# Kernel tuning notes

Measured on AMD Instinct MI355X. Metric: run time of the kernel, lower is better.

The kernel has to match this reference:

```python
import jax, jax.numpy as jnp
import numpy as np

E = 256
H = 512
LN_EPS = 1e-5
NORM_EPS = 1e-12


def setup_inputs() -> dict:
    key = jax.random.key(0)
    ks = jax.random.split(key, 8)
    B, N, M = 8, 128, 128
    track_features = jax.random.normal(ks[0], (B, N, E), dtype=jnp.float32)
    det_features = jax.random.normal(ks[1], (B, M, E), dtype=jnp.float32)
    # MLP params (torch Linear default init style: uniform, but values irrelevant for correctness harness)
    lim1 = 1.0 / np.sqrt(3 * E)
    W1 = jax.random.uniform(ks[2], (3 * E, H), minval=-lim1, maxval=lim1, dtype=jnp.float32)
    b1 = jax.random.uniform(ks[3], (H,), minval=-lim1, maxval=lim1, dtype=jnp.float32)
    gamma = jnp.ones((H,), dtype=jnp.float32)
    beta = jnp.zeros((H,), dtype=jnp.float32)
    lim2 = 1.0 / np.sqrt(H)
    W2 = jax.random.uniform(ks[4], (H, 1), minval=-lim2, maxval=lim2, dtype=jnp.float32)
    b2 = jax.random.uniform(ks[5], (1,), minval=-lim2, maxval=lim2, dtype=jnp.float32)
    return {"track_features": track_features, "det_features": det_features,
            "W1": W1, "b1": b1, "gamma": gamma, "beta": beta, "W2": W2, "b2": b2}


def _l2_normalize(x):
    # F.normalize(x, dim=-1): x / max(||x||_2, eps)
    n = jnp.sqrt(jnp.sum(x * x, axis=-1, keepdims=True))
    return x / jnp.maximum(n, NORM_EPS)


def reference(track_features, det_features, W1, b1, gamma, beta, W2, b2):
    t = _l2_normalize(track_features)   # (B, N, E)
    d = _l2_normalize(det_features)     # (B, M, E)
    tb = t[:, :, None, :]               # (B, N, 1, E)
    db = d[:, None, :, :]               # (B, 1, M, E)
    B, N, _ = t.shape
    M = d.shape[1]
    diff = jnp.abs(tb - db)                                  # (B, N, M, E)
    pair = jnp.concatenate([jnp.broadcast_to(tb, (B, N, M, E)),
                            jnp.broadcast_to(db, (B, N, M, E)),
                            diff], axis=-1)                  # (B, N, M, 3E)
    h = jnp.einsum('bnme,eh->bnmh', pair, W1) + b1           # (B, N, M, H)
    mu = jnp.mean(h, axis=-1, keepdims=True)
    var = jnp.mean((h - mu) ** 2, axis=-1, keepdims=True)
    h = (h - mu) * jax.lax.rsqrt(var + LN_EPS) * gamma + beta
    h = h * jax.nn.sigmoid(h)                                # SiLU
    out = jnp.einsum('bnmh,ho->bnmo', h, W2)[..., 0] + b2[0]  # (B, N, M)
    return out
```

## Files before the change

### kernel.cpp

```cpp
#include <hip/hip_runtime.h>
#include <hip/hip_bf16.h>
#include <cstdint>

typedef __bf16 bf16x8 __attribute__((ext_vector_type(8)));
typedef __bf16 bf16x2 __attribute__((ext_vector_type(2)));
typedef float f32x4 __attribute__((ext_vector_type(4)));

#define E_DIM 256
#define H_DIM 512
#define TSTR 260

static __device__ __forceinline__ unsigned pkbf(float a, float b) {
    bf16x2 h;
    h[0] = (__bf16)a;
    h[1] = (__bf16)b;
    return __builtin_bit_cast(unsigned, h);
}

__global__ __launch_bounds__(256)
void w1conv_kernel(const float* __restrict__ W1, __bf16* __restrict__ W1cc) {
    int u = blockIdx.x * 256 + threadIdx.x;
    int j   = u & 3;
    int h   = (u >> 2) & 511;
    int c   = (u >> 11) & 7;
    int mat = u >> 14;
    const float* src = W1 + (size_t)(mat * 256 + c * 32 + j * 8) * H_DIM + h;
    uint4 v;
    v.x = pkbf(src[0], src[(size_t)1 * H_DIM]);
    v.y = pkbf(src[(size_t)2 * H_DIM], src[(size_t)3 * H_DIM]);
    v.z = pkbf(src[(size_t)4 * H_DIM], src[(size_t)5 * H_DIM]);
    v.w = pkbf(src[(size_t)6 * H_DIM], src[(size_t)7 * H_DIM]);
    *(uint4*)(W1cc + ((size_t)(mat * 8 + c) * 512 + h) * 32 + j * 8) = v;
}

__global__ __launch_bounds__(512, 4)
void pq_mfma_kernel(const float* __restrict__ track, const float* __restrict__ det,
                    const __bf16* __restrict__ W1cc, const float* __restrict__ b1,
                    float* __restrict__ P, float* __restrict__ Q) {
    __shared__ __align__(16) __bf16 Ash[32 * 256];
    __shared__ float sclS[32];

    int tid  = threadIdx.x;
    int lane = tid & 63;
    int wave = tid >> 6;
    int lq   = lane >> 4;
    int lc   = lane & 15;

    int blk  = blockIdx.x;
    int mat  = blk >> 6;
    int rowg = (blk >> 1) & 31;
    int half = blk & 1;
    int r0   = rowg * 32;
    int h0   = half * 256;
    const float* src = mat ? det : track;

#pragma unroll
    for (int i = 0; i < 4; ++i) {
        int row = wave * 4 + i;
        float4 x = ((const float4*)(src + (size_t)(r0 + row) * E_DIM))[lane];
        float ss = x.x*x.x + x.y*x.y + x.z*x.z + x.w*x.w;
#pragma unroll
        for (int off = 32; off > 0; off >>= 1) ss += __shfl_xor(ss, off);
        if (lane == 0) sclS[row] = 1.0f / fmaxf(sqrtf(ss), 1e-12f);
    }
    __syncthreads();

#pragma unroll
    for (int r = 0; r < 2; ++r) {
        int row = r * 16 + lc;
        float st = sclS[row];
        const float* gp = src + (size_t)(r0 + row) * E_DIM + wave * 32 + lq * 8;
        float4 t0 = *(const float4*)gp;
        float4 t1 = *(const float4*)(gp + 4);
        uint4 v;
        v.x = pkbf(t0.x * st, t0.y * st);
        v.y = pkbf(t0.z * st, t0.w * st);
        v.z = pkbf(t1.x * st, t1.y * st);
        v.w = pkbf(t1.z * st, t1.w * st);
        *(uint4*)&Ash[(size_t)(r * 512 + wave * 64 + lane) * 8] = v;
    }
    __syncthreads();

    const uint4* Wg = (const uint4*)W1cc + (mat ? 16384 : 0);
    int hb = h0 + wave * 32 + lc;
    bf16x8 bwA[2], bwB[2];
#pragma unroll
    for (int ht = 0; ht < 2; ++ht)
        bwA[ht] = __builtin_bit_cast(bf16x8, Wg[(hb + ht * 16) * 4 + lq]);

    f32x4 acc[2][2];
#pragma unroll
    for (int pt = 0; pt < 2; ++pt)
#pragma unroll
        for (int ht = 0; ht < 2; ++ht)
            acc[pt][ht] = (f32x4){0.f, 0.f, 0.f, 0.f};

#pragma unroll 2
    for (int c = 0; c < 8; ++c) {
        bf16x8* cur = (c & 1) ? bwB : bwA;
        bf16x8* nxt = (c & 1) ? bwA : bwB;
        int c1 = (c + 1) & 7;
#pragma unroll
        for (int ht = 0; ht < 2; ++ht)
            nxt[ht] = __builtin_bit_cast(bf16x8, Wg[c1 * 2048 + (hb + ht * 16) * 4 + lq]);
#pragma unroll
        for (int pt = 0; pt < 2; ++pt) {
            bf16x8 af = *(const bf16x8*)&Ash[(size_t)((pt * 8 + c) * 64 + lane) * 8];
#pragma unroll
            for (int ht = 0; ht < 2; ++ht)
                acc[pt][ht] = __builtin_amdgcn_mfma_f32_16x16x32_bf16(cur[ht], af, acc[pt][ht], 0, 0, 0);
        }
    }

    float* dst = mat ? Q : P;
#pragma unroll
    for (int ht = 0; ht < 2; ++ht) {
        int h = h0 + wave * 32 + ht * 16 + lq * 4;
        f32x4 bvv = (f32x4){0.f, 0.f, 0.f, 0.f};
        if (!mat) bvv = *(const f32x4*)&b1[h];
#pragma unroll
        for (int pt = 0; pt < 2; ++pt) {
            f32x4 o = acc[pt][ht] + bvv;
            *(f32x4*)&dst[(size_t)(r0 + pt * 16 + lc) * H_DIM + h] = o;
        }
    }
}

__global__ __launch_bounds__(512, 4)
void main_kernel(const float* __restrict__ track, const float* __restrict__ det,
                 const __bf16* __restrict__ W1cc,
                 const float* __restrict__ P, const float* __restrict__ Q,
                 const float* __restrict__ gamma, const float* __restrict__ beta,
                 const float* __restrict__ W2, const float* __restrict__ b2,
                 float* __restrict__ out) {
    __shared__ __align__(16) char SMEM[49408];
    __bf16* Ash  = (__bf16*)SMEM;
    float*  tsl  = (float*)(SMEM + 32768);
    float*  dsl  = (float*)(SMEM + 41088);
    float*  LNr1 = (float*)(SMEM + 32768);
    float*  LNr2 = (float*)(SMEM + 35072);
    float*  Red2 = (float*)(SMEM + 37376);
    float*  MuS  = (float*)(SMEM + 39680);
    float*  RsS  = (float*)(SMEM + 39936);
    __shared__ float sclT[8], sclD[8];

    int tid  = threadIdx.x;
    int lane = tid & 63;
    int wave = tid >> 6;
    int lq   = lane >> 4;
    int lc   = lane & 15;

    int blk = blockIdx.x;
    int b   = blk >> 8;
    int n0  = ((blk >> 4) & 15) * 8;
    int m0  = (blk & 15) * 8;

    float4 tstage = ((const float4*)(track + (size_t)(b * 128 + n0 + wave) * E_DIM))[lane];
    float4 dstage = ((const float4*)(det   + (size_t)(b * 128 + m0 + wave) * E_DIM))[lane];

    const uint4* Wg = (const uint4*)W1cc + 32768;
    int hb = wave * 64 + lc;
    bf16x8 bwA[4], bwB[4];
#pragma unroll
    for (int ht = 0; ht < 4; ++ht)
        bwA[ht] = __builtin_bit_cast(bf16x8, Wg[(hb + ht * 16) * 4 + lq]);

    {
        float a = tstage.x*tstage.x + tstage.y*tstage.y + tstage.z*tstage.z + tstage.w*tstage.w;
        float d = dstage.x*dstage.x + dstage.y*dstage.y + dstage.z*dstage.z + dstage.w*dstage.w;
#pragma unroll
        for (int off = 32; off > 0; off >>= 1) { a += __shfl_xor(a, off); d += __shfl_xor(d, off); }
        if (lane == 0) {
            sclT[wave] = 1.0f / fmaxf(sqrtf(a), 1e-12f);
            sclD[wave] = 1.0f / fmaxf(sqrtf(d), 1e-12f);
        }
    }
    *(float4*)&tsl[wave * TSTR + lane * 4] = tstage;
    *(float4*)&dsl[wave * TSTR + lane * 4] = dstage;
    __syncthreads();

    {
        int k0 = wave * 32 + lq * 8;
        int ml = lane & 7;
        float sd = sclD[ml];
        const float* dr = dsl + ml * TSTR + k0;
        float4 d0 = *(const float4*)dr;
        float4 d1 = *(const float4*)(dr + 4);
#pragma unroll
        for (int r = 0; r < 4; ++r) {
            int nl = r * 2 + (lc >> 3);
            float st = sclT[nl];
            const float* tr = tsl + nl * TSTR + k0;
            float4 t0 = *(const float4*)tr;
            float4 t1 = *(const float4*)(tr + 4);
            uint4 v;
            v.x = pkbf(fabsf(t0.x * st - d0.x * sd), fabsf(t0.y * st - d0.y * sd));
            v.y = pkbf(fabsf(t0.z * st - d0.z * sd), fabsf(t0.w * st - d0.w * sd));
            v.z = pkbf(fabsf(t1.x * st - d1.x * sd), fabsf(t1.y * st - d1.y * sd));
            v.w = pkbf(fabsf(t1.z * st - d1.z * sd), fabsf(t1.w * st - d1.w * sd));
            *(uint4*)&Ash[(size_t)(r * 512 + wave * 64 + lane) * 8] = v;
        }
    }

    const float* Pb = P + (size_t)(b * 128 + n0) * H_DIM;
    const float* Qb = Q + (size_t)(b * 128 + m0) * H_DIM;
    f32x4 acc[4][4];
    {
        f32x4 qv[4];
#pragma unroll
        for (int ht = 0; ht < 4; ++ht)
            qv[ht] = *(const f32x4*)&Qb[(size_t)(lc & 7) * H_DIM + wave * 64 + ht * 16 + lq * 4];
#pragma unroll
        for (int pt = 0; pt < 4; ++pt) {
            int n = pt * 2 + (lc >> 3);
#pragma unroll
            for (int ht = 0; ht < 4; ++ht) {
                f32x4 pv = *(const f32x4*)&Pb[(size_t)n * H_DIM + wave * 64 + ht * 16 + lq * 4];
                acc[pt][ht] = pv + qv[ht];
            }
        }
    }
    __syncthreads();

#pragma unroll 2
    for (int c = 0; c < 8; ++c) {
        bf16x8* cur = (c & 1) ? bwB : bwA;
        bf16x8* nxt = (c & 1) ? bwA : bwB;
        int c1 = (c + 1) & 7;
#pragma unroll
        for (int ht = 0; ht < 4; ++ht)
            nxt[ht] = __builtin_bit_cast(bf16x8, Wg[c1 * 2048 + (hb + ht * 16) * 4 + lq]);
#pragma unroll
        for (int pt = 0; pt < 4; ++pt) {
            bf16x8 af = *(const bf16x8*)&Ash[(size_t)((pt * 8 + c) * 64 + lane) * 8];
#pragma unroll
            for (int ht = 0; ht < 4; ++ht)
                acc[pt][ht] = __builtin_amdgcn_mfma_f32_16x16x32_bf16(cur[ht], af, acc[pt][ht], 0, 0, 0);
        }
    }

#pragma unroll
    for (int pt = 0; pt < 4; ++pt) {
        float s1 = 0.f, s2 = 0.f;
#pragma unroll
        for (int ht = 0; ht < 4; ++ht)
#pragma unroll
            for (int rg = 0; rg < 4; ++rg) {
                float v = acc[pt][ht][rg];
                s1 += v; s2 += v * v;
            }
        s1 += __shfl_xor(s1, 16); s2 += __shfl_xor(s2, 16);
        s1 += __shfl_xor(s1, 32); s2 += __shfl_xor(s2, 32);
        if (lq == 0) {
            LNr1[(pt * 16 + lc) * 9 + wave] = s1;
            LNr2[(pt * 16 + lc) * 9 + wave] = s2;
        }
    }
    __syncthreads();
    if (tid < 64) {
        float S1 = 0.f, S2 = 0.f;
#pragma unroll
        for (int w = 0; w < 8; ++w) { S1 += LNr1[tid * 9 + w]; S2 += LNr2[tid * 9 + w]; }
        float mu = S1 * (1.0f / 512.0f);
        float var = S2 * (1.0f / 512.0f) - mu * mu;
        MuS[tid] = mu;
        RsS[tid] = rsqrtf(var + 1e-5f);
    }
    __syncthreads();

    float mus[4], rss[4];
#pragma unroll
    for (int pt = 0; pt < 4; ++pt) { mus[pt] = MuS[pt * 16 + lc]; rss[pt] = RsS[pt * 16 + lc]; }
    float ca[4] = {0.f, 0.f, 0.f, 0.f};
#pragma unroll
    for (int ht = 0; ht < 4; ++ht) {
        int h = wave * 64 + ht * 16 + lq * 4;
        f32x4 g  = *(const f32x4*)&gamma[h];
        f32x4 bb = *(const f32x4*)&beta[h];
        f32x4 w  = *(const f32x4*)&W2[h];
#pragma unroll
        for (int pt = 0; pt < 4; ++pt) {
#pragma unroll
            for (int rg = 0; rg < 4; ++rg) {
                float x = (acc[pt][ht][rg] - mus[pt]) * rss[pt] * g[rg] + bb[rg];
                float sg = __builtin_amdgcn_rcpf(1.0f + __expf(-x));
                ca[pt] += x * sg * w[rg];
            }
        }
    }
#pragma unroll
    for (int pt = 0; pt < 4; ++pt) {
        float c = ca[pt];
        c += __shfl_xor(c, 16);
        c += __shfl_xor(c, 32);
        if (lq == 0) Red2[(pt * 16 + lc) * 9 + wave] = c;
    }
    __syncthreads();
    if (tid < 64) {
        float o = b2[0];
#pragma unroll
        for (int w = 0; w < 8; ++w) o += Red2[tid * 9 + w];
        int n = n0 + (tid >> 3);
        int m = m0 + (tid & 7);
        out[(size_t)(b * 128 + n) * 128 + m] = o;
    }
}

extern "C" void kernel_launch(void* const* d_in, const int* in_sizes, int n_in,
                              void* d_out, int out_size, void* d_ws, size_t ws_size,
                              hipStream_t stream) {
    const float* track = (const float*)d_in[0];
    const float* det   = (const float*)d_in[1];
    const float* W1    = (const float*)d_in[2];
    const float* b1    = (const float*)d_in[3];
    const float* gamma = (const float*)d_in[4];
    const float* beta  = (const float*)d_in[5];
    const float* W2    = (const float*)d_in[6];
    const float* b2    = (const float*)d_in[7];
    float* out = (float*)d_out;

    char* ws = (char*)d_ws;
    float*  P     = (float*)(ws);
    float*  Q     = (float*)(ws + (2u << 20));
    __bf16* W1cc  = (__bf16*)(ws + (4u << 20));

    w1conv_kernel<<<192, 256, 0, stream>>>(W1, W1cc);
    pq_mfma_kernel<<<128, 512, 0, stream>>>(track, det, W1cc, b1, P, Q);
    main_kernel<<<2048, 512, 0, stream>>>(track, det, W1cc, P, Q, gamma, beta, W2, b2, out);
}
```

Baseline: 153.0 us.

## Switch main GEMM to 32x32x16 MFMA with new W1 diff-slice layout

Replaces the 16x16x32 bf16 MFMA tiling of the diff-feature GEMM with 32x32x16 MFMAs. A new W1 slice layout is added in the conversion kernel, and the LDS A-tile layout and accumulator mapping change to match. Normalization scales are applied before staging to LDS, so the diff build no longer reads per-row scales. The LN and output reductions are spread across all waves with shuffles instead of one wave looping. The larger MFMA should raise compute density and cut instruction count, at the cost of a deeper weight prefetch ring, more register pressure from f32x16 accumulators, and more conversion work.

Measured after the change: 163.4 us. 6.8% more time.

```diff
diff --git a/kernel.cpp b/kernel.cpp
--- a/kernel.cpp
+++ b/kernel.cpp
@@ -5,6 +5,7 @@
 typedef __bf16 bf16x8 __attribute__((ext_vector_type(8)));
 typedef __bf16 bf16x2 __attribute__((ext_vector_type(2)));
 typedef float f32x4 __attribute__((ext_vector_type(4)));
+typedef float f32x16 __attribute__((ext_vector_type(16)));
 
 #define E_DIM 256
 #define H_DIM 512
@@ -19,18 +20,37 @@
 
 __global__ __launch_bounds__(256)
 void w1conv_kernel(const float* __restrict__ W1, __bf16* __restrict__ W1cc) {
-    int u = blockIdx.x * 256 + threadIdx.x;
-    int j   = u & 3;
-    int h   = (u >> 2) & 511;
-    int c   = (u >> 11) & 7;
-    int mat = u >> 14;
-    const float* src = W1 + (size_t)(mat * 256 + c * 32 + j * 8) * H_DIM + h;
-    uint4 v;
-    v.x = pkbf(src[0], src[(size_t)1 * H_DIM]);
-    v.y = pkbf(src[(size_t)2 * H_DIM], src[(size_t)3 * H_DIM]);
-    v.z = pkbf(src[(size_t)4 * H_DIM], src[(size_t)5 * H_DIM]);
-    v.w = pkbf(src[(size_t)6 * H_DIM], src[(size_t)7 * H_DIM]);
-    *(uint4*)(W1cc + ((size_t)(mat * 8 + c) * 512 + h) * 32 + j * 8) = v;
+    int blk = blockIdx.x;
+    int tid = threadIdx.x;
+    if (blk < 128) {
+        int u = blk * 256 + tid;
+        int j   = u & 3;
+        int h   = (u >> 2) & 511;
+        int c   = (u >> 11) & 7;
+        int mat = u >> 14;
+        const float* src = W1 + (size_t)(mat * 256 + c * 32 + j * 8) * H_DIM + h;
+        uint4 v;
+        v.x = pkbf(src[0], src[(size_t)1 * H_DIM]);
+        v.y = pkbf(src[(size_t)2 * H_DIM], src[(size_t)3 * H_DIM]);
+        v.z = pkbf(src[(size_t)4 * H_DIM], src[(size_t)5 * H_DIM]);
+        v.w = pkbf(src[(size_t)6 * H_DIM], src[(size_t)7 * H_DIM]);
+        *(uint4*)(W1cc + ((size_t)(mat * 8 + c) * 512 + h) * 32 + j * 8) = v;
+    } else {
+        int v = (blk - 128) * 256 + tid;
+        int hh    = v & 31;
+        int k8    = (v >> 5) & 1;
+        int hgrp  = (v >> 6) & 15;
+        int kstep = v >> 10;
+        int h  = hgrp * 32 + hh;
+        int k0 = kstep * 16 + k8 * 8;
+        const float* src = W1 + (size_t)(512 + k0) * H_DIM + h;
+        uint4 o;
+        o.x = pkbf(src[0], src[(size_t)1 * H_DIM]);
+        o.y = pkbf(src[(size_t)2 * H_DIM], src[(size_t)3 * H_DIM]);
+        o.z = pkbf(src[(size_t)4 * H_DIM], src[(size_t)5 * H_DIM]);
+        o.w = pkbf(src[(size_t)6 * H_DIM], src[(size_t)7 * H_DIM]);
+        *(uint4*)(W1cc + 262144 + (size_t)v * 8) = o;
+    }
 }
 
 __global__ __launch_bounds__(512, 4)
@@ -142,13 +162,12 @@
     float*  Red2 = (float*)(SMEM + 37376);
     float*  MuS  = (float*)(SMEM + 39680);
     float*  RsS  = (float*)(SMEM + 39936);
-    __shared__ float sclT[8], sclD[8];
 
     int tid  = threadIdx.x;
     int lane = tid & 63;
     int wave = tid >> 6;
-    int lq   = lane >> 4;
-    int lc   = lane & 15;
+    int l32  = lane & 31;
+    int lh   = lane >> 5;
 
     int blk = blockIdx.x;
     int b   = blk >> 8;
@@ -158,151 +177,172 @@
     float4 tstage = ((const float4*)(track + (size_t)(b * 128 + n0 + wave) * E_DIM))[lane];
     float4 dstage = ((const float4*)(det   + (size_t)(b * 128 + m0 + wave) * E_DIM))[lane];
 
-    const uint4* Wg = (const uint4*)W1cc + 32768;
-    int hb = wave * 64 + lc;
-    bf16x8 bwA[4], bwB[4];
-#pragma unroll
-    for (int ht = 0; ht < 4; ++ht)
-        bwA[ht] = __builtin_bit_cast(bf16x8, Wg[(hb + ht * 16) * 4 + lq]);
+    const uint4* Wg2 = (const uint4*)W1cc + 32768;
+    bf16x8 bw[4][2];
+#pragma unroll
+    for (int ht = 0; ht < 2; ++ht) {
+        bw[0][ht] = __builtin_bit_cast(bf16x8, Wg2[(wave * 2 + ht) * 64 + lane]);
+        bw[1][ht] = __builtin_bit_cast(bf16x8, Wg2[(16 + wave * 2 + ht) * 64 + lane]);
+    }
 
     {
         float a = tstage.x*tstage.x + tstage.y*tstage.y + tstage.z*tstage.z + tstage.w*tstage.w;
         float d = dstage.x*dstage.x + dstage.y*dstage.y + dstage.z*dstage.z + dstage.w*dstage.w;
 #pragma unroll
         for (int off = 32; off > 0; off >>= 1) { a += __shfl_xor(a, off); d += __shfl_xor(d, off); }
-        if (lane == 0) {
-            sclT[wave] = 1.0f / fmaxf(sqrtf(a), 1e-12f);
-            sclD[wave] = 1.0f / fmaxf(sqrtf(d), 1e-12f);
-        }
+        float st = 1.0f / fmaxf(sqrtf(a), 1e-12f);
+        float sd = 1.0f / fmaxf(sqrtf(d), 1e-12f);
+        tstage.x *= st; tstage.y *= st; tstage.z *= st; tstage.w *= st;
+        dstage.x *= sd; dstage.y *= sd; dstage.z *= sd; dstage.w *= sd;
     }
     *(float4*)&tsl[wave * TSTR + lane * 4] = tstage;
     *(float4*)&dsl[wave * TSTR + lane * 4] = dstage;
     __syncthreads();
 
     {
-        int k0 = wave * 32 + lq * 8;
-        int ml = lane & 7;
-        float sd = sclD[ml];
-        const float* dr = dsl + ml * TSTR + k0;
-        float4 d0 = *(const float4*)dr;
-        float4 d1 = *(const float4*)(dr + 4);
-#pragma unroll
-        for (int r = 0; r < 4; ++r) {
-            int nl = r * 2 + (lc >> 3);
-            float st = sclT[nl];
-            const float* tr = tsl + nl * TSTR + k0;
-            float4 t0 = *(const float4*)tr;
-            float4 t1 = *(const float4*)(tr + 4);
+        int m   = l32;
+        int pt  = wave & 1;
+        int ks0 = wave >> 1;
+        int p   = pt * 32 + m;
+        const float* tr = tsl + (p >> 3) * TSTR;
+        const float* dr = dsl + (p & 7) * TSTR;
+#pragma unroll
+        for (int i = 0; i < 4; ++i) {
+            int kstep = i * 4 + ks0;
+            int k0 = kstep * 16 + lh * 8;
+            float4 t0 = *(const float4*)(tr + k0);
+            float4 t1 = *(const float4*)(tr + k0 + 4);
+            float4 d0 = *(const float4*)(dr + k0);
+            float4 d1 = *(const float4*)(dr + k0 + 4);
             uint4 v;
-            v.x = pkbf(fabsf(t0.x * st - d0.x * sd), fabsf(t0.y * st - d0.y * sd));
-            v.y = pkbf(fabsf(t0.z * st - d0.z * sd), fabsf(t0.w * st - d0.w * sd));
-            v.z = pkbf(fabsf(t1.x * st - d1.x * sd), fabsf(t1.y * st - d1.y * sd));
-            v.w = pkbf(fabsf(t1.z * st - d1.z * sd), fabsf(t1.w * st - d1.w * sd));
-            *(uint4*)&Ash[(size_t)(r * 512 + wave * 64 + lane) * 8] = v;
+            v.x = pkbf(fabsf(t0.x - d0.x), fabsf(t0.y - d0.y));
+            v.y = pkbf(fabsf(t0.z - d0.z), fabsf(t0.w - d0.w));
+            v.z = pkbf(fabsf(t1.x - d1.x), fabsf(t1.y - d1.y));
+            v.w = pkbf(fabsf(t1.z - d1.z), fabsf(t1.w - d1.w));
+            *(uint4*)&Ash[(size_t)(((kstep * 2 + pt) * 2 + lh) * 32 + m) * 8] = v;
         }
     }
 
     const float* Pb = P + (size_t)(b * 128 + n0) * H_DIM;
     const float* Qb = Q + (size_t)(b * 128 + m0) * H_DIM;
-    f32x4 acc[4][4];
-    {
-        f32x4 qv[4];
-#pragma unroll
-        for (int ht = 0; ht < 4; ++ht)
-            qv[ht] = *(const f32x4*)&Qb[(size_t)(lc & 7) * H_DIM + wave * 64 + ht * 16 + lq * 4];
-#pragma unroll
-        for (int pt = 0; pt < 4; ++pt) {
-            int n = pt * 2 + (lc >> 3);
-#pragma unroll
-            for (int ht = 0; ht < 4; ++ht) {
-                f32x4 pv = *(const f32x4*)&Pb[(size_t)n * H_DIM + wave * 64 + ht * 16 + lq * 4];
-                acc[pt][ht] = pv + qv[ht];
-            }
-        }
-    }
-    __syncthreads();
-
-#pragma unroll 2
-    for (int c = 0; c < 8; ++c) {
-        bf16x8* cur = (c & 1) ? bwB : bwA;
-        bf16x8* nxt = (c & 1) ? bwA : bwB;
-        int c1 = (c + 1) & 7;
-#pragma unroll
-        for (int ht = 0; ht < 4; ++ht)
-            nxt[ht] = __builtin_bit_cast(bf16x8, Wg[c1 * 2048 + (hb + ht * 16) * 4 + lq]);
-#pragma unroll
-        for (int pt = 0; pt < 4; ++pt) {
-            bf16x8 af = *(const bf16x8*)&Ash[(size_t)((pt * 8 + c) * 64 + lane) * 8];
-#pragma unroll
-            for (int ht = 0; ht < 4; ++ht)
-                acc[pt][ht] = __builtin_amdgcn_mfma_f32_16x16x32_bf16(cur[ht], af, acc[pt][ht], 0, 0, 0);
-        }
-    }
-
-#pragma unroll
-    for (int pt = 0; pt < 4; ++pt) {
+    f32x16 acc[2][2];
+    {
+        int mq = lane & 7;
+        f32x4 qv[2][4];
+#pragma unroll
+        for (int ht = 0; ht < 2; ++ht)
+#pragma unroll
+            for (int rq = 0; rq < 4; ++rq)
+                qv[ht][rq] = *(const f32x4*)&Qb[(size_t)mq * H_DIM + wave * 64 + ht * 32 + rq * 8 + lh * 4];
+#pragma unroll
+        for (int pt = 0; pt < 2; ++pt) {
+            int n = pt * 4 + (l32 >> 3);
+#pragma unroll
+            for (int ht = 0; ht < 2; ++ht)
+#pragma unroll
+                for (int rq = 0; rq < 4; ++rq) {
+                    f32x4 pv = *(const f32x4*)&Pb[(size_t)n * H_DIM + wave * 64 + ht * 32 + rq * 8 + lh * 4];
+                    f32x4 s = pv + qv[ht][rq];
+#pragma unroll
+                    for (int j = 0; j < 4; ++j) acc[pt][ht][rq * 4 + j] = s[j];
+                }
+        }
+    }
+    __syncthreads();
+
+#pragma unroll 4
+    for (int ks = 0; ks < 16; ++ks) {
+        if (ks < 14) {
+#pragma unroll
+            for (int ht = 0; ht < 2; ++ht)
+                bw[(ks + 2) & 3][ht] = __builtin_bit_cast(bf16x8,
+                    Wg2[((ks + 2) * 16 + wave * 2 + ht) * 64 + lane]);
+        }
+#pragma unroll
+        for (int pt = 0; pt < 2; ++pt) {
+            bf16x8 af = *(const bf16x8*)&Ash[(size_t)((ks * 2 + pt) * 64 + lane) * 8];
+#pragma unroll
+            for (int ht = 0; ht < 2; ++ht)
+                acc[pt][ht] = __builtin_amdgcn_mfma_f32_32x32x16_bf16(bw[ks & 3][ht], af, acc[pt][ht], 0, 0, 0);
+        }
+    }
+
+#pragma unroll
+    for (int pt = 0; pt < 2; ++pt) {
         float s1 = 0.f, s2 = 0.f;
 #pragma unroll
-        for (int ht = 0; ht < 4; ++ht)
-#pragma unroll
-            for (int rg = 0; rg < 4; ++rg) {
-                float v = acc[pt][ht][rg];
+        for (int ht = 0; ht < 2; ++ht)
+#pragma unroll
+            for (int r = 0; r < 16; ++r) {
+                float v = acc[pt][ht][r];
                 s1 += v; s2 += v * v;
             }
-        s1 += __shfl_xor(s1, 16); s2 += __shfl_xor(s2, 16);
         s1 += __shfl_xor(s1, 32); s2 += __shfl_xor(s2, 32);
-        if (lq == 0) {
-            LNr1[(pt * 16 + lc) * 9 + wave] = s1;
-            LNr2[(pt * 16 + lc) * 9 + wave] = s2;
-        }
-    }
-    __syncthreads();
-    if (tid < 64) {
-        float S1 = 0.f, S2 = 0.f;
-#pragma unroll
-        for (int w = 0; w < 8; ++w) { S1 += LNr1[tid * 9 + w]; S2 += LNr2[tid * 9 + w]; }
-        float mu = S1 * (1.0f / 512.0f);
-        float var = S2 * (1.0f / 512.0f) - mu * mu;
-        MuS[tid] = mu;
-        RsS[tid] = rsqrtf(var + 1e-5f);
-    }
-    __syncthreads();
-
-    float mus[4], rss[4];
-#pragma unroll
-    for (int pt = 0; pt < 4; ++pt) { mus[pt] = MuS[pt * 16 + lc]; rss[pt] = RsS[pt * 16 + lc]; }
-    float ca[4] = {0.f, 0.f, 0.f, 0.f};
-#pragma unroll
-    for (int ht = 0; ht < 4; ++ht) {
-        int h = wave * 64 + ht * 16 + lq * 4;
-        f32x4 g  = *(const f32x4*)&gamma[h];
-        f32x4 bb = *(const f32x4*)&beta[h];
-        f32x4 w  = *(const f32x4*)&W2[h];
-#pragma unroll
-        for (int pt = 0; pt < 4; ++pt) {
-#pragma unroll
-            for (int rg = 0; rg < 4; ++rg) {
-                float x = (acc[pt][ht][rg] - mus[pt]) * rss[pt] * g[rg] + bb[rg];
-                float sg = __builtin_amdgcn_rcpf(1.0f + __expf(-x));
-                ca[pt] += x * sg * w[rg];
+        if (lane < 32) {
+            LNr1[(pt * 32 + l32) * 9 + wave] = s1;
+            LNr2[(pt * 32 + l32) * 9 + wave] = s2;
+        }
+    }
+    __syncthreads();
+    {
+        int pair = wave * 8 + (lane >> 3);
+        int idx  = lane & 7;
+        float s1 = LNr1[pair * 9 + idx];
+        float s2 = LNr2[pair * 9 + idx];
+        s1 += __shfl_xor(s1, 1); s2 += __shfl_xor(s2, 1);
+        s1 += __shfl_xor(s1, 2); s2 += __shfl_xor(s2, 2);
+        s1 += __shfl_xor(s1, 4); s2 += __shfl_xor(s2, 4);
+        if ((lane & 7) == 0) {
+            float mu = s1 * (1.0f / 512.0f);
+            float var = s2 * (1.0f / 512.0f) - mu * mu;
+            MuS[pair] = mu;
+            RsS[pair] = rsqrtf(var + 1e-5f);
+        }
+    }
+    __syncthreads();
+
+    float mus[2], rss[2];
+#pragma unroll
+    for (int pt = 0; pt < 2; ++pt) { mus[pt] = MuS[pt * 32 + l32]; rss[pt] = RsS[pt * 32 + l32]; }
+    float ca[2] = {0.f, 0.f};
+#pragma unroll
+    for (int ht = 0; ht < 2; ++ht) {
+#pragma unroll
+        for (int rq = 0; rq < 4; ++rq) {
+            int h = wave * 64 + ht * 32 + rq * 8 + lh * 4;
+            f32x4 g  = *(const f32x4*)&gamma[h];
+            f32x4 bb = *(const f32x4*)&beta[h];
+            f32x4 w  = *(const f32x4*)&W2[h];
+#pragma unroll
+            for (int pt = 0; pt < 2; ++pt) {
+#pragma unroll
+                for (int j = 0; j < 4; ++j) {
+                    float x = (acc[pt][ht][rq * 4 + j] - mus[pt]) * rss[pt] * g[j] + bb[j];
+                    float sg = __builtin_amdgcn_rcpf(1.0f + __expf(-x));
+                    ca[pt] += x * sg * w[j];
+                }
             }
         }
     }
 #pragma unroll
-    for (int pt = 0; pt < 4; ++pt) {
+    for (int pt = 0; pt < 2; ++pt) {
         float c = ca[pt];
-        c += __shfl_xor(c, 16);
         c += __shfl_xor(c, 32);
-        if (lq == 0) Red2[(pt * 16 + lc) * 9 + wave] = c;
-    }
-    __syncthreads();
-    if (tid < 64) {
-        float o = b2[0];
-#pragma unroll
-        for (int w = 0; w < 8; ++w) o += Red2[tid * 9 + w];
-        int n = n0 + (tid >> 3);
-        int m = m0 + (tid & 7);
-        out[(size_t)(b * 128 + n) * 128 + m] = o;
+        if (lane < 32) Red2[(pt * 32 + l32) * 9 + wave] = c;
+    }
+    __syncthreads();
+    {
+        int pair = wave * 8 + (lane >> 3);
+        float c = Red2[pair * 9 + (lane & 7)];
+        c += __shfl_xor(c, 1);
+        c += __shfl_xor(c, 2);
+        c += __shfl_xor(c, 4);
+        if ((lane & 7) == 0) {
+            float o = c + b2[0];
+            int n = n0 + (pair >> 3);
+            int m = m0 + (pair & 7);
+            out[(size_t)(b * 128 + n) * 128 + m] = o;
+        }
     }
 }
 
```
